# Performance work log

Measured on AMD Instinct MI355X. Metric: run time of the kernel, lower is better.

Reference implementation:

```python
import jax, jax.numpy as jnp
import numpy as np

N = 50000       # nodes
E = 1_600_000   # edges (avg in-degree 32)
DE = 128        # edge feature dim
DN = 128        # node feature dim
DG = 128        # global feature dim
DH = 128        # MLP hidden
DO = 128        # MLP out (updated node dim)
DIN = DE + DN + DG


def setup_inputs() -> dict:
    key = jax.random.key(0)
    ks = jax.random.split(key, 8)
    return {
        "edge_attrs": jax.random.normal(ks[0], (E, DE), dtype=jnp.float32),
        "node_attrs": jax.random.normal(ks[1], (N, DN), dtype=jnp.float32),
        "global_attr": jax.random.normal(ks[2], (DG,), dtype=jnp.float32),
        "W1": jax.random.normal(ks[3], (DIN, DH), dtype=jnp.float32) * 0.05,
        "b1": jnp.zeros((DH,), dtype=jnp.float32),
        "W2": jax.random.normal(ks[4], (DH, DO), dtype=jnp.float32) * 0.05,
        "b2": jnp.zeros((DO,), dtype=jnp.float32),
        "edge_dst": jax.random.randint(ks[5], (E,), 0, N),  # receiver node id per edge
    }


def reference(edge_attrs, node_attrs, global_attr, W1, b1, W2, b2, edge_dst):
    # Mean-aggregate incoming edge attrs per destination node (segment mean).
    sums = jax.ops.segment_sum(edge_attrs, edge_dst, num_segments=N)          # [N, DE]
    cnt = jax.ops.segment_sum(
        jnp.ones((edge_dst.shape[0], 1), dtype=edge_attrs.dtype),
        edge_dst, num_segments=N)                                              # [N, 1]
    agg = sums / jnp.maximum(cnt, 1.0)
    # Concat [aggregated_edges, node_attr, global_attr] per node.
    g = jnp.broadcast_to(global_attr, (node_attrs.shape[0], global_attr.shape[0]))
    h = jnp.concatenate([agg, node_attrs, g], axis=-1)                         # [N, DIN]
    # Updater MLP.
    return jax.nn.relu(h @ W1 + b1) @ W2 + b2                                  # [N, DO]
```

## Files before the change

kernel.cpp:

```cpp
#include <hip/hip_runtime.h>
#include <hip/hip_bf16.h>


typedef __bf16 bf16x8 __attribute__((ext_vector_type(8)));
typedef float f32x4 __attribute__((ext_vector_type(4)));
typedef unsigned short ushort4v __attribute__((ext_vector_type(4)));

__device__ inline unsigned short f2bf(float f) {
    unsigned int u = __float_as_uint(f);
    u = u + 0x7fffu + ((u >> 16) & 1u);
    return (unsigned short)(u >> 16);
}

__global__ __launch_bounds__(256) void count_kernel(const int* __restrict__ dst,
                                                    int* __restrict__ cnt, int E) {
    int e = blockIdx.x * 256 + threadIdx.x;
    if (e < E) atomicAdd(&cnt[dst[e]], 1);
}

__global__ __launch_bounds__(1024) void scan_kernel(const int* __restrict__ cnt,
                                                    int* __restrict__ offs,
                                                    int* __restrict__ cursor, int n) {
    __shared__ int wsum[17];
    __shared__ int carry;
    int tid = threadIdx.x;
    int lane = tid & 63;
    int wv = tid >> 6;
    if (tid == 0) carry = 0;
    __syncthreads();
    for (int base = 0; base < n; base += 1024) {
        int idx = base + tid;
        int v = (idx < n) ? cnt[idx] : 0;
        int s = v;
        #pragma unroll
        for (int d = 1; d < 64; d <<= 1) {
            int t = __shfl_up(s, d, 64);
            if (lane >= d) s += t;
        }
        if (lane == 63) wsum[wv] = s;
        __syncthreads();
        if (tid == 0) {
            int run = 0;
            #pragma unroll
            for (int j = 0; j < 16; j++) { int t = wsum[j]; wsum[j] = run; run += t; }
            wsum[16] = run;
        }
        __syncthreads();
        int inc = s + wsum[wv];
        int exc = carry + inc - v;
        if (idx < n) { offs[idx] = exc; cursor[idx] = exc; }
        __syncthreads();
        if (tid == 0) carry += wsum[16];
        __syncthreads();
    }
}

__global__ __launch_bounds__(256) void scatter_kernel(const int* __restrict__ dst,
                                                      int* __restrict__ cursor,
                                                      int* __restrict__ eidl, int E) {
    int e = blockIdx.x * 256 + threadIdx.x;
    if (e < E) {
        int p = atomicAdd(&cursor[dst[e]], 1);
        eidl[p] = e;
    }
}

__global__ __launch_bounds__(256) void prep_kernel(const float* __restrict__ W1,
                                                   const float* __restrict__ b1,
                                                   const float* __restrict__ W2,
                                                   const float* __restrict__ g,
                                                   unsigned short* __restrict__ W1t,
                                                   unsigned short* __restrict__ W2t,
                                                   float* __restrict__ gvec) {
    int tid = blockIdx.x * blockDim.x + threadIdx.x;
    int stride = gridDim.x * blockDim.x;
    for (int i = tid; i < 128 * 256; i += stride) {
        int n = i >> 8, k = i & 255;
        W1t[i] = f2bf(W1[k * 128 + n]);
    }
    for (int i = tid; i < 128 * 128; i += stride) {
        int n = i >> 7, k = i & 127;
        W2t[i] = f2bf(W2[k * 128 + n]);
    }
    if (tid < 128) {
        float s = b1[tid];
        for (int k = 0; k < 128; k++) s += g[k] * W1[(256 + k) * 128 + tid];
        gvec[tid] = s;
    }
}

__global__ __launch_bounds__(256) void gather_kernel(const float* __restrict__ edge_attrs,
                                                     const int* __restrict__ eidl,
                                                     const int* __restrict__ offs,
                                                     const int* __restrict__ cnt,
                                                     float* __restrict__ agg, int n_nodes) {
    int gid = blockIdx.x * 256 + threadIdx.x;
    int n = gid >> 5, c = gid & 31;
    if (n >= n_nodes) return;
    int off = offs[n];
    int deg = cnt[n];
    const float4* ea = (const float4*)edge_attrs;
    float ax = 0.f, ay = 0.f, az = 0.f, aw = 0.f;
    int i = 0;
    for (; i + 4 <= deg; i += 4) {
        int e0 = eidl[off + i], e1 = eidl[off + i + 1];
        int e2 = eidl[off + i + 2], e3 = eidl[off + i + 3];
        float4 v0 = ea[e0 * 32 + c], v1 = ea[e1 * 32 + c];
        float4 v2 = ea[e2 * 32 + c], v3 = ea[e3 * 32 + c];
        ax += v0.x + v1.x + v2.x + v3.x;
        ay += v0.y + v1.y + v2.y + v3.y;
        az += v0.z + v1.z + v2.z + v3.z;
        aw += v0.w + v1.w + v2.w + v3.w;
    }
    for (; i < deg; i++) {
        int e = eidl[off + i];
        float4 v = ea[e * 32 + c];
        ax += v.x; ay += v.y; az += v.z; aw += v.w;
    }
    float inv = 1.0f / fmaxf((float)deg, 1.0f);
    float4 r; r.x = ax * inv; r.y = ay * inv; r.z = az * inv; r.w = aw * inv;
    ((float4*)agg)[n * 32 + c] = r;
}

#define LDH 264
#define LDY 136
__global__ __launch_bounds__(256) void mlp_kernel(const float* __restrict__ agg,
                                                  const float* __restrict__ node_attrs,
                                                  const unsigned short* __restrict__ W1t,
                                                  const unsigned short* __restrict__ W2t,
                                                  const float* __restrict__ gvec,
                                                  const float* __restrict__ b2,
                                                  float* __restrict__ out, int n_nodes) {
    __shared__ unsigned short lds_h[64 * LDH];
    __shared__ unsigned short lds_y[64 * LDY];
    int tid = threadIdx.x;
    int n0 = blockIdx.x * 64;

    for (int i = tid; i < 64 * 64; i += 256) {
        int r = i >> 6, c4 = i & 63;
        int node = n0 + r;
        float4 v; v.x = 0.f; v.y = 0.f; v.z = 0.f; v.w = 0.f;
        if (node < n_nodes) {
            if (c4 < 32) v = ((const float4*)agg)[node * 32 + c4];
            else         v = ((const float4*)node_attrs)[node * 32 + (c4 - 32)];
        }
        int col = c4 * 4;
        ushort4v u;
        u.x = f2bf(v.x); u.y = f2bf(v.y); u.z = f2bf(v.z); u.w = f2bf(v.w);
        *(ushort4v*)(lds_h + r * LDH + col) = u;
    }
    __syncthreads();

    int lane = tid & 63;
    int w = tid >> 6;
    int lrow = lane & 15;
    int quad = lane >> 4;
    int m = w * 16 + lrow;

    f32x4 acc[8];
    #pragma unroll
    for (int i = 0; i < 8; i++) acc[i] = (f32x4){0.f, 0.f, 0.f, 0.f};

    #pragma unroll
    for (int ks = 0; ks < 8; ks++) {
        bf16x8 a = *(const bf16x8*)(lds_h + m * LDH + ks * 32 + quad * 8);
        const unsigned short* bp = W1t + lrow * 256 + ks * 32 + quad * 8;
        #pragma unroll
        for (int nb = 0; nb < 8; nb++) {
            bf16x8 b = *(const bf16x8*)(bp + nb * 16 * 256);
            acc[nb] = __builtin_amdgcn_mfma_f32_16x16x32_bf16(a, b, acc[nb], 0, 0, 0);
        }
    }

    #pragma unroll
    for (int nb = 0; nb < 8; nb++) {
        int n = nb * 16 + lrow;
        float gv = gvec[n];
        #pragma unroll
        for (int reg = 0; reg < 4; reg++) {
            int row = w * 16 + quad * 4 + reg;
            float y = fmaxf(acc[nb][reg] + gv, 0.f);
            lds_y[row * LDY + n] = f2bf(y);
        }
    }
    __syncthreads();

    f32x4 acc2[8];
    #pragma unroll
    for (int i = 0; i < 8; i++) acc2[i] = (f32x4){0.f, 0.f, 0.f, 0.f};

    #pragma unroll
    for (int ks = 0; ks < 4; ks++) {
        bf16x8 a = *(const bf16x8*)(lds_y + m * LDY + ks * 32 + quad * 8);
        const unsigned short* bp = W2t + lrow * 128 + ks * 32 + quad * 8;
        #pragma unroll
        for (int nb = 0; nb < 8; nb++) {
            bf16x8 b = *(const bf16x8*)(bp + nb * 16 * 128);
            acc2[nb] = __builtin_amdgcn_mfma_f32_16x16x32_bf16(a, b, acc2[nb], 0, 0, 0);
        }
    }

    #pragma unroll
    for (int nb = 0; nb < 8; nb++) {
        int n = nb * 16 + lrow;
        float bb = b2[n];
        #pragma unroll
        for (int reg = 0; reg < 4; reg++) {
            int row = w * 16 + quad * 4 + reg;
            int node = n0 + row;
            if (node < n_nodes) out[node * 128 + n] = acc2[nb][reg] + bb;
        }
    }
}

extern "C" void kernel_launch(void* const* d_in, const int* in_sizes, int n_in,
                              void* d_out, int out_size, void* d_ws, size_t ws_size,
                              hipStream_t stream) {
    const float* edge_attrs  = (const float*)d_in[0];
    const float* node_attrs  = (const float*)d_in[1];
    const float* global_attr = (const float*)d_in[2];
    const float* W1 = (const float*)d_in[3];
    const float* b1 = (const float*)d_in[4];
    const float* W2 = (const float*)d_in[5];
    const float* b2 = (const float*)d_in[6];
    const int* edge_dst = (const int*)d_in[7];

    int E = in_sizes[0] / 128;
    int N = in_sizes[1] / 128;

    char* ws = (char*)d_ws;
    int* cnt    = (int*)ws;
    int* offs   = (int*)(ws + 0x40000);
    int* cursor = (int*)(ws + 0x80000);
    int* eidl   = (int*)(ws + 0xC0000);
    unsigned short* W1t = (unsigned short*)(ws + 0x800000);
    unsigned short* W2t = (unsigned short*)(ws + 0x810000);
    float* gvec = (float*)(ws + 0x818000);

    float* agg = (float*)d_out;
    float* out = (float*)d_out;

    hipMemsetAsync(cnt, 0, N * sizeof(int), stream);
    count_kernel<<<(E + 255) / 256, 256, 0, stream>>>(edge_dst, cnt, E);
    scan_kernel<<<1, 1024, 0, stream>>>(cnt, offs, cursor, N);
    scatter_kernel<<<(E + 255) / 256, 256, 0, stream>>>(edge_dst, cursor, eidl, E);
    prep_kernel<<<64, 256, 0, stream>>>(W1, b1, W2, global_attr, W1t, W2t, gvec);
    gather_kernel<<<(N * 32 + 255) / 256, 256, 0, stream>>>(edge_attrs, eidl, offs, cnt, agg, N);
    mlp_kernel<<<(N + 63) / 64, 256, 0, stream>>>(agg, node_attrs, W1t, W2t, gvec, b2, out, N);
}
```

Measured before the change: 1.389 ms.

## Parallelize scan, vectorize edge atomics, store bf16 aggregates, use nontemporal gathers

Replaces the single-block serial prefix scan with a three-pass multi-block scan, and makes count/scatter process four edges per thread via int4 loads. The gather loop is unrolled to 8 edges, uses nontemporal loads, and writes the mean aggregate directly as bf16 into workspace so the MLP load halves that traffic and skips conversion. Output stores are nontemporal. It adds kernel launches and relies on nontemporal hints helping the random gather.

```diff
diff --git a/kernel.cpp b/kernel.cpp
--- a/kernel.cpp
+++ b/kernel.cpp
@@ -5,6 +5,7 @@
 typedef __bf16 bf16x8 __attribute__((ext_vector_type(8)));
 typedef float f32x4 __attribute__((ext_vector_type(4)));
 typedef unsigned short ushort4v __attribute__((ext_vector_type(4)));
+typedef unsigned int uint4v __attribute__((ext_vector_type(4)));
 
 __device__ inline unsigned short f2bf(float f) {
     unsigned int u = __float_as_uint(f);
@@ -14,54 +15,103 @@
 
 __global__ __launch_bounds__(256) void count_kernel(const int* __restrict__ dst,
                                                     int* __restrict__ cnt, int E) {
-    int e = blockIdx.x * 256 + threadIdx.x;
-    if (e < E) atomicAdd(&cnt[dst[e]], 1);
-}
-
-__global__ __launch_bounds__(1024) void scan_kernel(const int* __restrict__ cnt,
+    int t = blockIdx.x * 256 + threadIdx.x;
+    int base = t * 4;
+    if (base + 3 < E) {
+        int4 d = *(const int4*)(dst + base);
+        atomicAdd(&cnt[d.x], 1);
+        atomicAdd(&cnt[d.y], 1);
+        atomicAdd(&cnt[d.z], 1);
+        atomicAdd(&cnt[d.w], 1);
+    } else {
+        for (int e = base; e < E; e++) atomicAdd(&cnt[dst[e]], 1);
+    }
+}
+
+__global__ __launch_bounds__(256) void scan1_kernel(const int* __restrict__ cnt,
+                                                    int* __restrict__ bsum, int n) {
+    __shared__ int ws[4];
+    int tid = threadIdx.x;
+    int idx = blockIdx.x * 256 + tid;
+    int v = (idx < n) ? cnt[idx] : 0;
+    #pragma unroll
+    for (int d = 32; d > 0; d >>= 1) v += __shfl_down(v, d, 64);
+    if ((tid & 63) == 0) ws[tid >> 6] = v;
+    __syncthreads();
+    if (tid == 0) bsum[blockIdx.x] = ws[0] + ws[1] + ws[2] + ws[3];
+}
+
+__global__ __launch_bounds__(256) void scan2_kernel(const int* __restrict__ bsum,
+                                                    int* __restrict__ bscan, int nb) {
+    __shared__ int ws[4];
+    int tid = threadIdx.x;
+    int lane = tid & 63, wv = tid >> 6;
+    int v = (tid < nb) ? bsum[tid] : 0;
+    int s = v;
+    #pragma unroll
+    for (int d = 1; d < 64; d <<= 1) {
+        int t = __shfl_up(s, d, 64);
+        if (lane >= d) s += t;
+    }
+    if (lane == 63) ws[wv] = s;
+    __syncthreads();
+    if (tid == 0) {
+        int run = 0;
+        #pragma unroll
+        for (int j = 0; j < 4; j++) { int t = ws[j]; ws[j] = run; run += t; }
+    }
+    __syncthreads();
+    int exc = s - v + ws[wv];
+    if (tid < nb) bscan[tid] = exc;
+}
+
+__global__ __launch_bounds__(256) void scan3_kernel(const int* __restrict__ cnt,
+                                                    const int* __restrict__ bscan,
                                                     int* __restrict__ offs,
                                                     int* __restrict__ cursor, int n) {
-    __shared__ int wsum[17];
-    __shared__ int carry;
+    __shared__ int ws[4];
     int tid = threadIdx.x;
-    int lane = tid & 63;
-    int wv = tid >> 6;
-    if (tid == 0) carry = 0;
-    __syncthreads();
-    for (int base = 0; base < n; base += 1024) {
-        int idx = base + tid;
-        int v = (idx < n) ? cnt[idx] : 0;
-        int s = v;
-        #pragma unroll
-        for (int d = 1; d < 64; d <<= 1) {
-            int t = __shfl_up(s, d, 64);
-            if (lane >= d) s += t;
-        }
-        if (lane == 63) wsum[wv] = s;
-        __syncthreads();
-        if (tid == 0) {
-            int run = 0;
-            #pragma unroll
-            for (int j = 0; j < 16; j++) { int t = wsum[j]; wsum[j] = run; run += t; }
-            wsum[16] = run;
-        }
-        __syncthreads();
-        int inc = s + wsum[wv];
-        int exc = carry + inc - v;
-        if (idx < n) { offs[idx] = exc; cursor[idx] = exc; }
-        __syncthreads();
-        if (tid == 0) carry += wsum[16];
-        __syncthreads();
-    }
+    int idx = blockIdx.x * 256 + tid;
+    int lane = tid & 63, wv = tid >> 6;
+    int v = (idx < n) ? cnt[idx] : 0;
+    int s = v;
+    #pragma unroll
+    for (int d = 1; d < 64; d <<= 1) {
+        int t = __shfl_up(s, d, 64);
+        if (lane >= d) s += t;
+    }
+    if (lane == 63) ws[wv] = s;
+    __syncthreads();
+    if (tid == 0) {
+        int run = 0;
+        #pragma unroll
+        for (int j = 0; j < 4; j++) { int t = ws[j]; ws[j] = run; run += t; }
+    }
+    __syncthreads();
+    int exc = s - v + ws[wv] + bscan[blockIdx.x];
+    if (idx < n) { offs[idx] = exc; cursor[idx] = exc; }
 }
 
 __global__ __launch_bounds__(256) void scatter_kernel(const int* __restrict__ dst,
                                                       int* __restrict__ cursor,
                                                       int* __restrict__ eidl, int E) {
-    int e = blockIdx.x * 256 + threadIdx.x;
-    if (e < E) {
-        int p = atomicAdd(&cursor[dst[e]], 1);
-        eidl[p] = e;
+    int t = blockIdx.x * 256 + threadIdx.x;
+    int base = t * 4;
+    if (base + 3 < E) {
+        int4 d = *(const int4*)(dst + base);
+        int p0 = atomicAdd(&cursor[d.x], 1);
+        int p1 = atomicAdd(&cursor[d.y], 1);
+        int p2 = atomicAdd(&cursor[d.z], 1);
+        int p3 = atomicAdd(&cursor[d.w], 1);
+        eidl[p0] = base;
+        eidl[p1] = base + 1;
+        eidl[p2] = base + 2;
+        eidl[p3] = base + 3;
+    } else {
+        for (int e = base; e < E; e++) {
+            int p = atomicAdd(&cursor[dst[e]], 1);
+            eidl[p] = e;
+        }
     }
 }
 
@@ -93,20 +143,33 @@
                                                      const int* __restrict__ eidl,
                                                      const int* __restrict__ offs,
                                                      const int* __restrict__ cnt,
-                                                     float* __restrict__ agg, int n_nodes) {
+                                                     unsigned short* __restrict__ aggbf,
+                                                     int n_nodes) {
     int gid = blockIdx.x * 256 + threadIdx.x;
     int n = gid >> 5, c = gid & 31;
     if (n >= n_nodes) return;
     int off = offs[n];
     int deg = cnt[n];
-    const float4* ea = (const float4*)edge_attrs;
+    const f32x4* ea = (const f32x4*)edge_attrs;
     float ax = 0.f, ay = 0.f, az = 0.f, aw = 0.f;
     int i = 0;
+    for (; i + 8 <= deg; i += 8) {
+        int e[8];
+        #pragma unroll
+        for (int j = 0; j < 8; j++) e[j] = eidl[off + i + j];
+        #pragma unroll
+        for (int j = 0; j < 8; j++) {
+            f32x4 v = __builtin_nontemporal_load(&ea[e[j] * 32 + c]);
+            ax += v.x; ay += v.y; az += v.z; aw += v.w;
+        }
+    }
     for (; i + 4 <= deg; i += 4) {
         int e0 = eidl[off + i], e1 = eidl[off + i + 1];
         int e2 = eidl[off + i + 2], e3 = eidl[off + i + 3];
-        float4 v0 = ea[e0 * 32 + c], v1 = ea[e1 * 32 + c];
-        float4 v2 = ea[e2 * 32 + c], v3 = ea[e3 * 32 + c];
+        f32x4 v0 = __builtin_nontemporal_load(&ea[e0 * 32 + c]);
+        f32x4 v1 = __builtin_nontemporal_load(&ea[e1 * 32 + c]);
+        f32x4 v2 = __builtin_nontemporal_load(&ea[e2 * 32 + c]);
+        f32x4 v3 = __builtin_nontemporal_load(&ea[e3 * 32 + c]);
         ax += v0.x + v1.x + v2.x + v3.x;
         ay += v0.y + v1.y + v2.y + v3.y;
         az += v0.z + v1.z + v2.z + v3.z;
@@ -114,17 +177,19 @@
     }
     for (; i < deg; i++) {
         int e = eidl[off + i];
-        float4 v = ea[e * 32 + c];
+        f32x4 v = __builtin_nontemporal_load(&ea[e * 32 + c]);
         ax += v.x; ay += v.y; az += v.z; aw += v.w;
     }
     float inv = 1.0f / fmaxf((float)deg, 1.0f);
-    float4 r; r.x = ax * inv; r.y = ay * inv; r.z = az * inv; r.w = aw * inv;
-    ((float4*)agg)[n * 32 + c] = r;
+    ushort4v u;
+    u.x = f2bf(ax * inv); u.y = f2bf(ay * inv);
+    u.z = f2bf(az * inv); u.w = f2bf(aw * inv);
+    *(ushort4v*)(aggbf + n * 128 + c * 4) = u;
 }
 
 #define LDH 264
 #define LDY 136
-__global__ __launch_bounds__(256) void mlp_kernel(const float* __restrict__ agg,
+__global__ __launch_bounds__(256) void mlp_kernel(const unsigned short* __restrict__ aggbf,
                                                   const float* __restrict__ node_attrs,
                                                   const unsigned short* __restrict__ W1t,
                                                   const unsigned short* __restrict__ W2t,
@@ -136,18 +201,21 @@
     int tid = threadIdx.x;
     int n0 = blockIdx.x * 64;
 
-    for (int i = tid; i < 64 * 64; i += 256) {
-        int r = i >> 6, c4 = i & 63;
+    for (int i = tid; i < 64 * 16; i += 256) {
+        int r = i >> 4, c8 = i & 15;
         int node = n0 + r;
-        float4 v; v.x = 0.f; v.y = 0.f; v.z = 0.f; v.w = 0.f;
-        if (node < n_nodes) {
-            if (c4 < 32) v = ((const float4*)agg)[node * 32 + c4];
-            else         v = ((const float4*)node_attrs)[node * 32 + (c4 - 32)];
-        }
-        int col = c4 * 4;
+        uint4v u = (uint4v){0u, 0u, 0u, 0u};
+        if (node < n_nodes) u = ((const uint4v*)aggbf)[node * 16 + c8];
+        *(uint4v*)(lds_h + r * LDH + c8 * 8) = u;
+    }
+    for (int i = tid; i < 64 * 32; i += 256) {
+        int r = i >> 5, c4 = i & 31;
+        int node = n0 + r;
+        f32x4 v = (f32x4){0.f, 0.f, 0.f, 0.f};
+        if (node < n_nodes) v = __builtin_nontemporal_load(&((const f32x4*)node_attrs)[node * 32 + c4]);
         ushort4v u;
         u.x = f2bf(v.x); u.y = f2bf(v.y); u.z = f2bf(v.z); u.w = f2bf(v.w);
-        *(ushort4v*)(lds_h + r * LDH + col) = u;
+        *(ushort4v*)(lds_h + r * LDH + 128 + c4 * 4) = u;
     }
     __syncthreads();
 
@@ -208,7 +276,8 @@
         for (int reg = 0; reg < 4; reg++) {
             int row = w * 16 + quad * 4 + reg;
             int node = n0 + row;
-            if (node < n_nodes) out[node * 128 + n] = acc2[nb][reg] + bb;
+            if (node < n_nodes)
+                __builtin_nontemporal_store(acc2[nb][reg] + bb, &out[node * 128 + n]);
         }
     }
 }
@@ -236,15 +305,21 @@
     unsigned short* W1t = (unsigned short*)(ws + 0x800000);
     unsigned short* W2t = (unsigned short*)(ws + 0x810000);
     float* gvec = (float*)(ws + 0x818000);
-
-    float* agg = (float*)d_out;
+    int* bsum   = (int*)(ws + 0x820000);
+    int* bscan  = (int*)(ws + 0x821000);
+    unsigned short* aggbf = (unsigned short*)(ws + 0x900000);
+
     float* out = (float*)d_out;
 
+    int NB = (N + 255) / 256;
+
     hipMemsetAsync(cnt, 0, N * sizeof(int), stream);
-    count_kernel<<<(E + 255) / 256, 256, 0, stream>>>(edge_dst, cnt, E);
-    scan_kernel<<<1, 1024, 0, stream>>>(cnt, offs, cursor, N);
-    scatter_kernel<<<(E + 255) / 256, 256, 0, stream>>>(edge_dst, cursor, eidl, E);
+    count_kernel<<<(E / 4 + 255) / 256, 256, 0, stream>>>(edge_dst, cnt, E);
+    scan1_kernel<<<NB, 256, 0, stream>>>(cnt, bsum, N);
+    scan2_kernel<<<1, 256, 0, stream>>>(bsum, bscan, NB);
+    scan3_kernel<<<NB, 256, 0, stream>>>(cnt, bscan, offs, cursor, N);
+    scatter_kernel<<<(E / 4 + 255) / 256, 256, 0, stream>>>(edge_dst, cursor, eidl, E);
     prep_kernel<<<64, 256, 0, stream>>>(W1, b1, W2, global_attr, W1t, W2t, gvec);
-    gather_kernel<<<(N * 32 + 255) / 256, 256, 0, stream>>>(edge_attrs, eidl, offs, cnt, agg, N);
-    mlp_kernel<<<(N + 63) / 64, 256, 0, stream>>>(agg, node_attrs, W1t, W2t, gvec, b2, out, N);
-}
+    gather_kernel<<<(N * 32 + 255) / 256, 256, 0, stream>>>(edge_attrs, eidl, offs, cnt, aggbf, N);
+    mlp_kernel<<<(N + 63) / 64, 256, 0, stream>>>(aggbf, node_attrs, W1t, W2t, gvec, b2, out, N);
+}
```

After: 1.292 ms. 7.0% less time.
